# Kernel optimization log

Hardware: AMD Instinct MI355X
Metric: run time of the kernel (lower is better)

Reference implementation:

```python
import jax, jax.numpy as jnp
import numpy as np

N_SRC = 50000
N_DST = 50000
N_EDGES = 500000
HIDDEN = 128
HEADS = 8
HEAD_DIM = HIDDEN // HEADS
SCALE = HEAD_DIM ** -0.5


def setup_inputs() -> dict:
    key = jax.random.key(0)
    ks = jax.random.split(key, 12)
    lim = 1.0 / np.sqrt(HIDDEN)
    def lin(k):
        kw, kb = jax.random.split(k)
        W = jax.random.uniform(kw, (HIDDEN, HIDDEN), jnp.float32, -lim, lim)
        b = jax.random.uniform(kb, (HIDDEN,), jnp.float32, -lim, lim)
        return W, b
    Wq, bq = lin(ks[0]); Wk, bk = lin(ks[1]); Wv, bv = lin(ks[2]); Wo, bo = lin(ks[3])
    return {
        "x_src": jax.random.normal(ks[4], (N_SRC, HIDDEN), jnp.float32),
        "x_dst": jax.random.normal(ks[5], (N_DST, HIDDEN), jnp.float32),
        "edge_index": jax.random.randint(ks[6], (2, N_EDGES), 0, N_SRC, jnp.int64),
        "Wq": Wq, "bq": bq, "Wk": Wk, "bk": bk, "Wv": Wv, "bv": bv,
        "Wo": Wo, "bo": bo,
        "edge_bias": jax.random.normal(ks[7], (HEADS,), jnp.float32) * 0.02,
    }


def reference(x_src, x_dst, edge_index, Wq, bq, Wk, bk, Wv, bv, Wo, bo, edge_bias):
    num_dst = x_dst.shape[0]
    # projections (torch Linear: y = x W^T + b), reshape to (N, H, D)
    q = (x_dst @ Wq.T + bq).reshape(num_dst, HEADS, HEAD_DIM)
    k = (x_src @ Wk.T + bk).reshape(-1, HEADS, HEAD_DIM)
    v = (x_src @ Wv.T + bv).reshape(-1, HEADS, HEAD_DIM)
    src_idx, dst_idx = edge_index[0], edge_index[1]
    # per-edge dot-product scores: (E, H)
    scores = (q[dst_idx] * k[src_idx]).sum(-1) * SCALE + edge_bias
    # sparse softmax over edges grouped by destination
    m = jax.ops.segment_max(scores, dst_idx, num_segments=num_dst)  # (N_dst, H)
    e = jnp.exp(scores - m[dst_idx])
    s = jax.ops.segment_sum(e, dst_idx, num_segments=num_dst)  # (N_dst, H)
    w = e / (s[dst_idx] + 1e-8)  # (E, H)
    # scatter-add aggregate weighted values
    out = jax.ops.segment_sum(w[:, :, None] * v[src_idx], dst_idx, num_segments=num_dst)
    out = out.reshape(num_dst, HIDDEN)
    return out @ Wo.T + bo
```

## Files before the change

### kernel.cpp

```cpp
#include <hip/hip_runtime.h>
#include <math.h>

#define HIDDEN 128
#define SCALE 0.25f
#define NB_F 256

typedef __attribute__((ext_vector_type(8))) short short8v;
typedef __attribute__((ext_vector_type(4))) float f32x4;

__device__ __forceinline__ unsigned short f2bf(float f) {
  const unsigned u = __float_as_uint(f);
  const unsigned r = u + 0x7fffu + ((u >> 16) & 1u);
  return (unsigned short)(r >> 16);
}
__device__ __forceinline__ unsigned pack_bf2(float a, float b) {
  unsigned r;
  asm("v_cvt_pk_bf16_f32 %0, %1, %2" : "=v"(r) : "v"(a), "v"(b));
  return r;
}
__device__ __forceinline__ float bflo(unsigned u) { return __uint_as_float(u << 16); }
__device__ __forceinline__ float bfhi(unsigned u) { return __uint_as_float(u & 0xffff0000u); }

__device__ __forceinline__ void gload_lds16(const void* g, void* l) {
  __builtin_amdgcn_global_load_lds(
      (const __attribute__((address_space(1))) unsigned*)g,
      (__attribute__((address_space(3))) unsigned*)l, 16, 0, 0);
}

__global__ __launch_bounds__(256) void init_kernel(
    const float* __restrict__ W0, const float* __restrict__ W1,
    const float* __restrict__ W2, const float* __restrict__ W3,
    unsigned short* __restrict__ Wfrag, int* __restrict__ zero_base, int nzero4)
{
  if (blockIdx.x < 32) {
    const int chunk = blockIdx.x * 256 + threadIdx.x;
    const int m = chunk >> 11;
    const int rem = chunk & 2047;
    const int l = rem & 63;
    const int nkk = rem >> 6;
    const int n = nkk >> 2, kk = nkk & 3;
    const float* W = (m == 0) ? W0 : (m == 1) ? W1 : (m == 2) ? W2 : W3;
    const int row = n * 16 + (l & 15);
    const int k0 = kk * 32 + (l >> 4) * 8;
    const float4 v0 = *(const float4*)&W[row * 128 + k0];
    const float4 v1 = *(const float4*)&W[row * 128 + k0 + 4];
    uint4 o;
    o.x = (unsigned)f2bf(v0.x) | ((unsigned)f2bf(v0.y) << 16);
    o.y = (unsigned)f2bf(v0.z) | ((unsigned)f2bf(v0.w) << 16);
    o.z = (unsigned)f2bf(v1.x) | ((unsigned)f2bf(v1.y) << 16);
    o.w = (unsigned)f2bf(v1.z) | ((unsigned)f2bf(v1.w) << 16);
    *(uint4*)&Wfrag[(size_t)chunk * 8] = o;
  } else {
    const int idx4 = (blockIdx.x - 32) * 256 + threadIdx.x;
    if (idx4 < nzero4)
      *(int4*)&zero_base[idx4 * 4] = make_int4(0, 0, 0, 0);
  }
}

__global__ __launch_bounds__(256, 4) void qkv_count_kernel(
    const float* __restrict__ x_src, const float* __restrict__ x_dst,
    const unsigned short* __restrict__ Wfrag,
    const float* __restrict__ bq, const float* __restrict__ bk,
    const float* __restrict__ bv,
    unsigned short* __restrict__ qb, unsigned short* __restrict__ kvb,
    int Nsrc, int Ndst,
    const int* __restrict__ ei, int E, int* __restrict__ counts, int cblocks)
{
  __shared__ __align__(16) char WsB[32768];
  __shared__ float bias_s[128];
  const int t = threadIdx.x;
  int bid = blockIdx.x;

  if (bid < cblocks) {
    const int e = (bid * 256 + t) * 4;
    if (e + 4 <= E) {
      const int4 d = *(const int4*)&ei[E + e];
      atomicAdd(&counts[d.x], 1);
      atomicAdd(&counts[d.y], 1);
      atomicAdd(&counts[d.z], 1);
      atomicAdd(&counts[d.w], 1);
    } else {
      for (int k = e; k < E; ++k) atomicAdd(&counts[ei[E + k]], 1);
    }
    return;
  }
  bid -= cblocks;

  const int flavor = bid / NB_F, sub = bid % NB_F;
  const float* X; const float* bias; const unsigned short* wbase;
  unsigned short* out; int ostride, ooff, N;
  if (flavor == 0)      { X = x_src; bias = bk; wbase = Wfrag + 16384; out = kvb; ostride = 256; ooff = 0;   N = Nsrc; }
  else if (flavor == 1) { X = x_src; bias = bv; wbase = Wfrag + 32768; out = kvb; ostride = 256; ooff = 128; N = Nsrc; }
  else                  { X = x_dst; bias = bq; wbase = Wfrag;         out = qb;  ostride = 128; ooff = 0;   N = Ndst; }

  #pragma unroll
  for (int it = 0; it < 8; ++it) {
    const int off = (it * 256 + t) * 16;
    gload_lds16((const char*)wbase + off, WsB + off);
  }
  if (t < 128) bias_s[t] = bias[t];
  asm volatile("s_waitcnt vmcnt(0)" ::: "memory");
  __syncthreads();

  const int l = t & 63, w = t >> 6;
  const int r16 = l & 15, g16 = l >> 4;
  const int ntiles = (N + 15) >> 4;
  const int stride = NB_F * 4;
  int tile = sub * 4 + w;
  if (tile >= ntiles) return;

  float4 xv[8];
  {
    const int row = tile * 16 + r16;
    const bool valid = row < N;
    const float* xp = X + (size_t)row * 128 + g16 * 8;
    #pragma unroll
    for (int kk = 0; kk < 4; ++kk) {
      xv[2 * kk]     = valid ? *(const float4*)(xp + kk * 32)     : make_float4(0.f, 0.f, 0.f, 0.f);
      xv[2 * kk + 1] = valid ? *(const float4*)(xp + kk * 32 + 4) : make_float4(0.f, 0.f, 0.f, 0.f);
    }
  }
  for (; tile < ntiles; tile += stride) {
    const int nt = tile + stride;
    short8v a[4];
    #pragma unroll
    for (int kk = 0; kk < 4; ++kk) {
      uint4 u;
      u.x = pack_bf2(xv[2 * kk].x,     xv[2 * kk].y);
      u.y = pack_bf2(xv[2 * kk].z,     xv[2 * kk].w);
      u.z = pack_bf2(xv[2 * kk + 1].x, xv[2 * kk + 1].y);
      u.w = pack_bf2(xv[2 * kk + 1].z, xv[2 * kk + 1].w);
      a[kk] = *(short8v*)&u;
    }
    if (nt < ntiles) {
      const int row = nt * 16 + r16;
      const bool valid = row < N;
      const float* xp = X + (size_t)row * 128 + g16 * 8;
      #pragma unroll
      for (int kk = 0; kk < 4; ++kk) {
        xv[2 * kk]     = valid ? *(const float4*)(xp + kk * 32)     : make_float4(0.f, 0.f, 0.f, 0.f);
        xv[2 * kk + 1] = valid ? *(const float4*)(xp + kk * 32 + 4) : make_float4(0.f, 0.f, 0.f, 0.f);
      }
    }
    f32x4 acc[8];
    #pragma unroll
    for (int n = 0; n < 8; ++n) acc[n] = (f32x4){0.f, 0.f, 0.f, 0.f};
    #pragma unroll
    for (int kk = 0; kk < 4; ++kk) {
      #pragma unroll
      for (int n = 0; n < 8; ++n) {
        const short8v wf = *(const short8v*)&WsB[((n * 4 + kk) * 64 + l) * 16];
        acc[n] = __builtin_amdgcn_mfma_f32_16x16x32_bf16(wf, a[kk], acc[n], 0, 0, 0);
      }
    }
    const int row = tile * 16 + r16;
    if (row < N) {
      unsigned short* orow = out + (size_t)row * ostride + ooff;
      #pragma unroll
      for (int n = 0; n < 8; ++n) {
        const float4 bb = *(const float4*)&bias_s[n * 16 + g16 * 4];
        uint2 o;
        o.x = pack_bf2(acc[n][0] + bb.x, acc[n][1] + bb.y);
        o.y = pack_bf2(acc[n][2] + bb.z, acc[n][3] + bb.w);
        *(uint2*)&orow[n * 16 + g16 * 4] = o;
      }
    }
  }
}

__global__ __launch_bounds__(256, 4) void out_gemm_kernel(
    const unsigned short* __restrict__ agg, const unsigned short* __restrict__ Wfrag_o,
    const float* __restrict__ bo, float* __restrict__ Y, int N)
{
  __shared__ __align__(16) char WsB[32768];
  __shared__ float bias_s[128];
  const int t = threadIdx.x;
  #pragma unroll
  for (int it = 0; it < 8; ++it) {
    const int off = (it * 256 + t) * 16;
    gload_lds16((const char*)Wfrag_o + off, WsB + off);
  }
  if (t < 128) bias_s[t] = bo[t];
  asm volatile("s_waitcnt vmcnt(0)" ::: "memory");
  __syncthreads();

  const int l = t & 63, w = t >> 6;
  const int r16 = l & 15, g16 = l >> 4;
  const int ntiles = (N + 15) >> 4;
  const int stride = NB_F * 4;
  int tile = blockIdx.x * 4 + w;
  if (tile >= ntiles) return;

  uint4 av[4];
  {
    const int row = tile * 16 + r16;
    const bool valid = row < N;
    const unsigned short* ap = agg + (size_t)row * 128 + g16 * 8;
    #pragma unroll
    for (int kk = 0; kk < 4; ++kk)
      av[kk] = valid ? *(const uint4*)(ap + kk * 32) : make_uint4(0, 0, 0, 0);
  }
  for (; tile < ntiles; tile += stride) {
    const int nt = tile + stride;
    short8v a[4];
    #pragma unroll
    for (int kk = 0; kk < 4; ++kk) a[kk] = *(short8v*)&av[kk];
    if (nt < ntiles) {
      const int row = nt * 16 + r16;
      const bool valid = row < N;
      const unsigned short* ap = agg + (size_t)row * 128 + g16 * 8;
      #pragma unroll
      for (int kk = 0; kk < 4; ++kk)
        av[kk] = valid ? *(const uint4*)(ap + kk * 32) : make_uint4(0, 0, 0, 0);
    }
    f32x4 acc[8];
    #pragma unroll
    for (int n = 0; n < 8; ++n) acc[n] = (f32x4){0.f, 0.f, 0.f, 0.f};
    #pragma unroll
    for (int kk = 0; kk < 4; ++kk) {
      #pragma unroll
      for (int n = 0; n < 8; ++n) {
        const short8v wf = *(const short8v*)&WsB[((n * 4 + kk) * 64 + l) * 16];
        acc[n] = __builtin_amdgcn_mfma_f32_16x16x32_bf16(wf, a[kk], acc[n], 0, 0, 0);
      }
    }
    const int row = tile * 16 + r16;
    if (row < N) {
      float* yrow = Y + (size_t)row * 128;
      #pragma unroll
      for (int n = 0; n < 8; ++n) {
        const float4 bb = *(const float4*)&bias_s[n * 16 + g16 * 4];
        *(float4*)&yrow[n * 16 + g16 * 4] =
            make_float4(acc[n][0] + bb.x, acc[n][1] + bb.y, acc[n][2] + bb.z, acc[n][3] + bb.w);
      }
    }
  }
}

__global__ __launch_bounds__(256) void scan_fused_kernel(
    const int* __restrict__ counts, int n, int* __restrict__ bsums,
    int* __restrict__ done, int* __restrict__ offsets)
{
  const int b = blockIdx.x, t = threadIdx.x;
  const int lane = t & 63, wid = t >> 6;
  const int idx = b * 256 + t;
  const int x = (idx < n) ? counts[idx] : 0;
  int v = x;
  #pragma unroll
  for (int off = 1; off < 64; off <<= 1) {
    const int tmp = __shfl_up(v, off);
    if (lane >= off) v += tmp;
  }
  __shared__ int wsum[4];
  __shared__ int base_s;
  if (lane == 63) wsum[wid] = v;
  __syncthreads();
  if (t == 0) {
    bsums[b] = wsum[0] + wsum[1] + wsum[2] + wsum[3];
    __threadfence();
    atomicAdd(done, 1);
    while (atomicAdd(done, 0) < (int)gridDim.x) {}
  }
  __syncthreads();
  __threadfence();
  int pre = (t < b) ? bsums[t] : 0;
  #pragma unroll
  for (int off = 1; off < 64; off <<= 1) pre += __shfl_xor(pre, off);
  __shared__ int pres[4];
  if (lane == 0) pres[wid] = pre;
  __syncthreads();
  if (t == 0) base_s = pres[0] + pres[1] + pres[2] + pres[3];
  __syncthreads();
  int wbase = 0;
  for (int p = 0; p < wid; ++p) wbase += wsum[p];
  if (idx < n) offsets[idx] = base_s + wbase + v - x;
}

__global__ __launch_bounds__(256) void scatter_kernel(
    const int* __restrict__ ei, int E, int* __restrict__ offsets,
    int* __restrict__ csr_src)
{
  const int e = (blockIdx.x * 256 + threadIdx.x) * 4;
  if (e + 4 <= E) {
    const int4 s = *(const int4*)&ei[e];
    const int4 d = *(const int4*)&ei[E + e];
    int p;
    p = atomicAdd(&offsets[d.x], 1); csr_src[p] = s.x;
    p = atomicAdd(&offsets[d.y], 1); csr_src[p] = s.y;
    p = atomicAdd(&offsets[d.z], 1); csr_src[p] = s.z;
    p = atomicAdd(&offsets[d.w], 1); csr_src[p] = s.w;
  } else {
    for (int k = e; k < E; ++k) {
      const int d = ei[E + k];
      const int p = atomicAdd(&offsets[d], 1);
      csr_src[p] = ei[k];
    }
  }
}

__global__ __launch_bounds__(256) void edge_attn_kernel(
    const unsigned short* __restrict__ qb, const unsigned short* __restrict__ kvb,
    const float* __restrict__ eb, const int* __restrict__ offsets,
    const int* __restrict__ counts, const int* __restrict__ csr_src,
    unsigned short* __restrict__ agg, int Ndst)
{
  const int wave = blockIdx.x * 4 + (threadIdx.x >> 6);
  if (wave >= Ndst) return;
  const int lane = threadIdx.x & 63;
  const int eg = lane >> 3, h = lane & 7;

  const uint4 q0 = *(const uint4*)&qb[(size_t)wave * 128 + h * 16];
  const uint4 q1 = *(const uint4*)&qb[(size_t)wave * 128 + h * 16 + 8];
  const float bias = eb[h];
  const int ro = (wave == 0) ? 0 : offsets[wave - 1];
  const int cnt = counts[wave];

  float acc[16];
  #pragma unroll
  for (int j = 0; j < 16; ++j) acc[j] = 0.f;
  float s = 0.f;

  const int iters = (cnt + 7) >> 3;
  int eA = eg;
  bool actA = eA < cnt;
  int srcA = actA ? csr_src[ro + eA] : 0;
  size_t baseA = (size_t)srcA * 256 + h * 16;
  uint4 kA0 = *(const uint4*)&kvb[baseA];
  uint4 kA1 = *(const uint4*)&kvb[baseA + 8];
  uint4 vA0 = *(const uint4*)&kvb[baseA + 128];
  uint4 vA1 = *(const uint4*)&kvb[baseA + 136];
  int eB = eA + 8;
  bool actB = eB < cnt;
  int srcB = actB ? csr_src[ro + eB] : 0;

  for (int it = 0; it < iters; ++it) {
    const size_t baseB = (size_t)srcB * 256 + h * 16;
    const uint4 kB0 = *(const uint4*)&kvb[baseB];
    const uint4 kB1 = *(const uint4*)&kvb[baseB + 8];
    const uint4 vB0 = *(const uint4*)&kvb[baseB + 128];
    const uint4 vB1 = *(const uint4*)&kvb[baseB + 136];
    const int eC = eB + 8;
    const bool actC = eC < cnt;
    const int srcC = actC ? csr_src[ro + eC] : 0;

    float p = 0.f;
    p = fmaf(bflo(q0.x), bflo(kA0.x), p); p = fmaf(bfhi(q0.x), bfhi(kA0.x), p);
    p = fmaf(bflo(q0.y), bflo(kA0.y), p); p = fmaf(bfhi(q0.y), bfhi(kA0.y), p);
    p = fmaf(bflo(q0.z), bflo(kA0.z), p); p = fmaf(bfhi(q0.z), bfhi(kA0.z), p);
    p = fmaf(bflo(q0.w), bflo(kA0.w), p); p = fmaf(bfhi(q0.w), bfhi(kA0.w), p);
    p = fmaf(bflo(q1.x), bflo(kA1.x), p); p = fmaf(bfhi(q1.x), bfhi(kA1.x), p);
    p = fmaf(bflo(q1.y), bflo(kA1.y), p); p = fmaf(bfhi(q1.y), bfhi(kA1.y), p);
    p = fmaf(bflo(q1.z), bflo(kA1.z), p); p = fmaf(bfhi(q1.z), bfhi(kA1.z), p);
    p = fmaf(bflo(q1.w), bflo(kA1.w), p); p = fmaf(bfhi(q1.w), bfhi(kA1.w), p);

    const float wgt = actA ? __expf(fmaf(p, SCALE, bias)) : 0.f;
    s += wgt;
    acc[0]  = fmaf(wgt, bflo(vA0.x), acc[0]);  acc[1]  = fmaf(wgt, bfhi(vA0.x), acc[1]);
    acc[2]  = fmaf(wgt, bflo(vA0.y), acc[2]);  acc[3]  = fmaf(wgt, bfhi(vA0.y), acc[3]);
    acc[4]  = fmaf(wgt, bflo(vA0.z), acc[4]);  acc[5]  = fmaf(wgt, bfhi(vA0.z), acc[5]);
    acc[6]  = fmaf(wgt, bflo(vA0.w), acc[6]);  acc[7]  = fmaf(wgt, bfhi(vA0.w), acc[7]);
    acc[8]  = fmaf(wgt, bflo(vA1.x), acc[8]);  acc[9]  = fmaf(wgt, bfhi(vA1.x), acc[9]);
    acc[10] = fmaf(wgt, bflo(vA1.y), acc[10]); acc[11] = fmaf(wgt, bfhi(vA1.y), acc[11]);
    acc[12] = fmaf(wgt, bflo(vA1.z), acc[12]); acc[13] = fmaf(wgt, bfhi(vA1.z), acc[13]);
    acc[14] = fmaf(wgt, bflo(vA1.w), acc[14]); acc[15] = fmaf(wgt, bfhi(vA1.w), acc[15]);

    kA0 = kB0; kA1 = kB1; vA0 = vB0; vA1 = vB1;
    actA = actB; actB = actC; srcB = srcC; eB = eC;
  }

  const bool b0 = eg & 1, b1 = (eg >> 1) & 1, b2 = (eg >> 2) & 1;
  float r8[8];
  #pragma unroll
  for (int j = 0; j < 8; ++j) {
    const float keep = b0 ? acc[j + 8] : acc[j];
    const float send = b0 ? acc[j] : acc[j + 8];
    r8[j] = keep + __shfl_xor(send, 8);
  }
  float r4[4];
  #pragma unroll
  for (int j = 0; j < 4; ++j) {
    const float keep = b1 ? r8[j + 4] : r8[j];
    const float send = b1 ? r8[j] : r8[j + 4];
    r4[j] = keep + __shfl_xor(send, 16);
  }
  float r2[2];
  #pragma unroll
  for (int j = 0; j < 2; ++j) {
    const float keep = b2 ? r4[j + 2] : r4[j];
    const float send = b2 ? r4[j] : r4[j + 2];
    r2[j] = keep + __shfl_xor(send, 32);
  }
  s += __shfl_xor(s, 8); s += __shfl_xor(s, 16); s += __shfl_xor(s, 32);
  const float rs = 1.0f / (s + 1e-8f);
  const int col = h * 16 + (b0 ? 8 : 0) + (b1 ? 4 : 0) + (b2 ? 2 : 0);
  *(unsigned*)&agg[(size_t)wave * 128 + col] = pack_bf2(r2[0] * rs, r2[1] * rs);
}

extern "C" void kernel_launch(void* const* d_in, const int* in_sizes, int n_in,
                              void* d_out, int out_size, void* d_ws, size_t ws_size,
                              hipStream_t stream) {
  const float* x_src = (const float*)d_in[0];
  const float* x_dst = (const float*)d_in[1];
  const int*   ei    = (const int*)d_in[2];
  const float* Wq = (const float*)d_in[3];
  const float* bq = (const float*)d_in[4];
  const float* Wk = (const float*)d_in[5];
  const float* bk = (const float*)d_in[6];
  const float* Wv = (const float*)d_in[7];
  const float* bv = (const float*)d_in[8];
  const float* Wo = (const float*)d_in[9];
  const float* bo = (const float*)d_in[10];
  const float* eb = (const float*)d_in[11];

  const int Nsrc = in_sizes[0] / HIDDEN;
  const int Ndst = in_sizes[1] / HIDDEN;
  const int E    = in_sizes[2] / 2;

  char* w = (char*)d_ws;
  unsigned short* qb   = (unsigned short*)w; w += (size_t)Ndst * 128 * 2;
  unsigned short* kvb  = (unsigned short*)w; w += (size_t)Nsrc * 256 * 2;
  unsigned short* aggb = (unsigned short*)w; w += (size_t)Ndst * 128 * 2;
  unsigned short* Wb   = (unsigned short*)w; w += (size_t)4 * 16384 * 2;
  int* counts  = (int*)w; w += (size_t)Ndst * sizeof(int);
  int* done    = (int*)w; w += 64 * sizeof(int);
  int* offsets = (int*)w; w += (size_t)Ndst * sizeof(int);
  int* bsums   = (int*)w; w += 256 * sizeof(int);
  int* csr_src = (int*)w; w += (size_t)E * sizeof(int);

  dim3 blk256(256);
  const int nzero4 = (Ndst + 64 + 3) / 4;
  const int zblocks = (nzero4 + 255) / 256;
  init_kernel<<<32 + zblocks, blk256, 0, stream>>>(Wq, Wk, Wv, Wo, Wb, counts, nzero4);

  const int e4blocks = (E / 4 + 255) / 256;
  qkv_count_kernel<<<e4blocks + 3 * NB_F, blk256, 0, stream>>>(
      x_src, x_dst, Wb, bq, bk, bv, qb, kvb, Nsrc, Ndst, ei, E, counts, e4blocks);

  const int nb = (Ndst + 255) / 256;
  scan_fused_kernel<<<nb, blk256, 0, stream>>>(counts, Ndst, bsums, done, offsets);

  scatter_kernel<<<e4blocks, blk256, 0, stream>>>(ei, E, offsets, csr_src);

  const int ablocks = (Ndst + 3) / 4;
  edge_attn_kernel<<<ablocks, blk256, 0, stream>>>(qb, kvb, eb, offsets, counts,
                                                   csr_src, aggb, Ndst);

  out_gemm_kernel<<<NB_F, blk256, 0, stream>>>(aggb, Wb + 49152, bo, (float*)d_out, Ndst);
}
```

Before: 170.3 us.

## Keep weight fragments in registers and stage activations through swizzled double-buffered LDS

Both projection GEMM kernels now hold all 32 weight MFMA fragments in VGPRs instead of LDS. Activation tiles of 64 rows per block are staged through a double-buffered, XOR-swizzled LDS buffer: coalesced fp32 loads converted to bf16 for QKV, and global_load_lds for the output GEMM. Bias is folded into the accumulator init, and the edge-count blocks move after the GEMM blocks. The aim is to cut LDS weight reads and improve load coalescing, at the cost of higher register pressure (occupancy hint lowered from 4 to 2) and fewer GEMM blocks per type.

```diff
diff --git a/kernel.cpp b/kernel.cpp
--- a/kernel.cpp
+++ b/kernel.cpp
@@ -3,7 +3,8 @@
 
 #define HIDDEN 128
 #define SCALE 0.25f
-#define NB_F 256
+#define NB_TYPE 170
+#define NB_O 256
 
 typedef __attribute__((ext_vector_type(8))) short short8v;
 typedef __attribute__((ext_vector_type(4))) float f32x4;
@@ -57,22 +58,21 @@
   }
 }
 
-__global__ __launch_bounds__(256, 4) void qkv_count_kernel(
+__global__ __launch_bounds__(256, 2) void qkv_gemm_count_kernel(
     const float* __restrict__ x_src, const float* __restrict__ x_dst,
     const unsigned short* __restrict__ Wfrag,
     const float* __restrict__ bq, const float* __restrict__ bk,
     const float* __restrict__ bv,
     unsigned short* __restrict__ qb, unsigned short* __restrict__ kvb,
     int Nsrc, int Ndst,
-    const int* __restrict__ ei, int E, int* __restrict__ counts, int cblocks)
-{
-  __shared__ __align__(16) char WsB[32768];
-  __shared__ float bias_s[128];
+    const int* __restrict__ ei, int E, int* __restrict__ counts)
+{
+  __shared__ __align__(16) char Xs[2][16384];
   const int t = threadIdx.x;
   int bid = blockIdx.x;
 
-  if (bid < cblocks) {
-    const int e = (bid * 256 + t) * 4;
+  if (bid >= 3 * NB_TYPE) {
+    const int e = ((bid - 3 * NB_TYPE) * 256 + t) * 4;
     if (e + 4 <= E) {
       const int4 d = *(const int4*)&ei[E + e];
       atomicAdd(&counts[d.x], 1);
@@ -84,156 +84,156 @@
     }
     return;
   }
-  bid -= cblocks;
-
-  const int flavor = bid / NB_F, sub = bid % NB_F;
+
+  const int l = t & 63, w = t >> 6;
+  const int r16 = l & 15, g16 = l >> 4;
+
   const float* X; const float* bias; const unsigned short* wbase;
   unsigned short* out; int ostride, ooff, N;
-  if (flavor == 0)      { X = x_src; bias = bk; wbase = Wfrag + 16384; out = kvb; ostride = 256; ooff = 0;   N = Nsrc; }
-  else if (flavor == 1) { X = x_src; bias = bv; wbase = Wfrag + 32768; out = kvb; ostride = 256; ooff = 128; N = Nsrc; }
-  else                  { X = x_dst; bias = bq; wbase = Wfrag;         out = qb;  ostride = 128; ooff = 0;   N = Ndst; }
-
-  #pragma unroll
-  for (int it = 0; it < 8; ++it) {
-    const int off = (it * 256 + t) * 16;
-    gload_lds16((const char*)wbase + off, WsB + off);
-  }
-  if (t < 128) bias_s[t] = bias[t];
-  asm volatile("s_waitcnt vmcnt(0)" ::: "memory");
-  __syncthreads();
-
+  if (bid < NB_TYPE)          { X = x_src; bias = bk; wbase = Wfrag + 16384; out = kvb; ostride = 256; ooff = 0;   N = Nsrc; }
+  else if (bid < 2 * NB_TYPE) { bid -= NB_TYPE;   X = x_src; bias = bv; wbase = Wfrag + 32768; out = kvb; ostride = 256; ooff = 128; N = Nsrc; }
+  else                        { bid -= 2 * NB_TYPE; X = x_dst; bias = bq; wbase = Wfrag;       out = qb;  ostride = 128; ooff = 0;   N = Ndst; }
+  const int ntiles = (N + 63) >> 6;
+
+  short8v wfr[32];
+  #pragma unroll
+  for (int i = 0; i < 32; ++i) wfr[i] = ((const short8v*)wbase)[i * 64 + l];
+
+  const int srow = l >> 5;
+  const int scol = (l & 31) * 4;
+
+  float4 xv[8];
+  int tile = bid;
+  {
+    #pragma unroll
+    for (int j = 0; j < 8; ++j) {
+      const int r = j * 2 + srow;
+      const int g = tile * 64 + w * 16 + r;
+      xv[j] = make_float4(0.f, 0.f, 0.f, 0.f);
+      if (g < N) xv[j] = *(const float4*)&X[(size_t)g * 128 + scol];
+    }
+    #pragma unroll
+    for (int j = 0; j < 8; ++j) {
+      const int r = j * 2 + srow;
+      uint2 p;
+      p.x = pack_bf2(xv[j].x, xv[j].y);
+      p.y = pack_bf2(xv[j].z, xv[j].w);
+      *(uint2*)&Xs[0][(w * 16 + r) * 256 + ((scol * 2) ^ ((r & 7) << 4))] = p;
+    }
+  }
+  int cur = 0;
+  for (; tile < ntiles; tile += NB_TYPE) {
+    const int nt = tile + NB_TYPE;
+    if (nt < ntiles) {
+      #pragma unroll
+      for (int j = 0; j < 8; ++j) {
+        const int r = j * 2 + srow;
+        const int g = nt * 64 + w * 16 + r;
+        xv[j] = make_float4(0.f, 0.f, 0.f, 0.f);
+        if (g < N) xv[j] = *(const float4*)&X[(size_t)g * 128 + scol];
+      }
+    }
+    f32x4 acc[8];
+    #pragma unroll
+    for (int n = 0; n < 8; ++n) {
+      const float4 bb = *(const float4*)&bias[n * 16 + g16 * 4];
+      acc[n] = (f32x4){bb.x, bb.y, bb.z, bb.w};
+    }
+    const char* ax = &Xs[cur][(w * 16 + r16) * 256];
+    #pragma unroll
+    for (int kk = 0; kk < 4; ++kk) {
+      const short8v b = *(const short8v*)(ax + ((kk * 64 + g16 * 16) ^ ((r16 & 7) << 4)));
+      #pragma unroll
+      for (int n = 0; n < 8; ++n)
+        acc[n] = __builtin_amdgcn_mfma_f32_16x16x32_bf16(wfr[n * 4 + kk], b, acc[n], 0, 0, 0);
+    }
+    const int grow = tile * 64 + w * 16 + r16;
+    if (grow < N) {
+      unsigned short* orow = out + (size_t)grow * ostride + ooff;
+      #pragma unroll
+      for (int n = 0; n < 8; ++n) {
+        uint2 o;
+        o.x = pack_bf2(acc[n][0], acc[n][1]);
+        o.y = pack_bf2(acc[n][2], acc[n][3]);
+        *(uint2*)&orow[n * 16 + g16 * 4] = o;
+      }
+    }
+    if (nt < ntiles) {
+      #pragma unroll
+      for (int j = 0; j < 8; ++j) {
+        const int r = j * 2 + srow;
+        uint2 p;
+        p.x = pack_bf2(xv[j].x, xv[j].y);
+        p.y = pack_bf2(xv[j].z, xv[j].w);
+        *(uint2*)&Xs[cur ^ 1][(w * 16 + r) * 256 + ((scol * 2) ^ ((r & 7) << 4))] = p;
+      }
+    }
+    cur ^= 1;
+  }
+}
+
+__global__ __launch_bounds__(256, 2) void out_gemm_kernel(
+    const unsigned short* __restrict__ agg, const unsigned short* __restrict__ Wo_frag,
+    const float* __restrict__ bo, float* __restrict__ Y, int N)
+{
+  __shared__ __align__(16) char Xs[2][16384];
+  const int t = threadIdx.x;
   const int l = t & 63, w = t >> 6;
   const int r16 = l & 15, g16 = l >> 4;
-  const int ntiles = (N + 15) >> 4;
-  const int stride = NB_F * 4;
-  int tile = sub * 4 + w;
-  if (tile >= ntiles) return;
-
-  float4 xv[8];
+  const int ntiles = (N + 63) >> 6;
+
+  short8v wfr[32];
+  #pragma unroll
+  for (int i = 0; i < 32; ++i) wfr[i] = ((const short8v*)Wo_frag)[i * 64 + l];
+
+  int tile = blockIdx.x;
   {
-    const int row = tile * 16 + r16;
-    const bool valid = row < N;
-    const float* xp = X + (size_t)row * 128 + g16 * 8;
+    #pragma unroll
+    for (int it = 0; it < 4; ++it) {
+      const int row16 = it * 4 + (l >> 4);
+      const int grow = tile * 64 + w * 16 + row16;
+      const int sb = ((l & 15) * 16) ^ ((row16 & 7) << 4);
+      gload_lds16((const char*)agg + (size_t)grow * 256 + sb,
+                  &Xs[0][w * 4096 + it * 1024 + l * 16]);
+    }
+  }
+  int cur = 0;
+  for (; tile < ntiles; tile += NB_O) {
+    const int nt = tile + NB_O;
+    asm volatile("s_waitcnt vmcnt(0)" ::: "memory");
+    __builtin_amdgcn_sched_barrier(0);
+    if (nt < ntiles) {
+      #pragma unroll
+      for (int it = 0; it < 4; ++it) {
+        const int row16 = it * 4 + (l >> 4);
+        const int grow = nt * 64 + w * 16 + row16;
+        const int sb = ((l & 15) * 16) ^ ((row16 & 7) << 4);
+        gload_lds16((const char*)agg + (size_t)grow * 256 + sb,
+                    &Xs[cur ^ 1][w * 4096 + it * 1024 + l * 16]);
+      }
+    }
+    f32x4 acc[8];
+    #pragma unroll
+    for (int n = 0; n < 8; ++n) {
+      const float4 bb = *(const float4*)&bo[n * 16 + g16 * 4];
+      acc[n] = (f32x4){bb.x, bb.y, bb.z, bb.w};
+    }
+    const char* ax = &Xs[cur][(w * 16 + r16) * 256];
     #pragma unroll
     for (int kk = 0; kk < 4; ++kk) {
-      xv[2 * kk]     = valid ? *(const float4*)(xp + kk * 32)     : make_float4(0.f, 0.f, 0.f, 0.f);
-      xv[2 * kk + 1] = valid ? *(const float4*)(xp + kk * 32 + 4) : make_float4(0.f, 0.f, 0.f, 0.f);
-    }
-  }
-  for (; tile < ntiles; tile += stride) {
-    const int nt = tile + stride;
-    short8v a[4];
-    #pragma unroll
-    for (int kk = 0; kk < 4; ++kk) {
-      uint4 u;
-      u.x = pack_bf2(xv[2 * kk].x,     xv[2 * kk].y);
-      u.y = pack_bf2(xv[2 * kk].z,     xv[2 * kk].w);
-      u.z = pack_bf2(xv[2 * kk + 1].x, xv[2 * kk + 1].y);
-      u.w = pack_bf2(xv[2 * kk + 1].z, xv[2 * kk + 1].w);
-      a[kk] = *(short8v*)&u;
-    }
-    if (nt < ntiles) {
-      const int row = nt * 16 + r16;
-      const bool valid = row < N;
-      const float* xp = X + (size_t)row * 128 + g16 * 8;
-      #pragma unroll
-      for (int kk = 0; kk < 4; ++kk) {
-        xv[2 * kk]     = valid ? *(const float4*)(xp + kk * 32)     : make_float4(0.f, 0.f, 0.f, 0.f);
-        xv[2 * kk + 1] = valid ? *(const float4*)(xp + kk * 32 + 4) : make_float4(0.f, 0.f, 0.f, 0.f);
-      }
-    }
-    f32x4 acc[8];
-    #pragma unroll
-    for (int n = 0; n < 8; ++n) acc[n] = (f32x4){0.f, 0.f, 0.f, 0.f};
-    #pragma unroll
-    for (int kk = 0; kk < 4; ++kk) {
-      #pragma unroll
-      for (int n = 0; n < 8; ++n) {
-        const short8v wf = *(const short8v*)&WsB[((n * 4 + kk) * 64 + l) * 16];
-        acc[n] = __builtin_amdgcn_mfma_f32_16x16x32_bf16(wf, a[kk], acc[n], 0, 0, 0);
-      }
-    }
-    const int row = tile * 16 + r16;
-    if (row < N) {
-      unsigned short* orow = out + (size_t)row * ostride + ooff;
-      #pragma unroll
-      for (int n = 0; n < 8; ++n) {
-        const float4 bb = *(const float4*)&bias_s[n * 16 + g16 * 4];
-        uint2 o;
-        o.x = pack_bf2(acc[n][0] + bb.x, acc[n][1] + bb.y);
-        o.y = pack_bf2(acc[n][2] + bb.z, acc[n][3] + bb.w);
-        *(uint2*)&orow[n * 16 + g16 * 4] = o;
-      }
-    }
-  }
-}
-
-__global__ __launch_bounds__(256, 4) void out_gemm_kernel(
-    const unsigned short* __restrict__ agg, const unsigned short* __restrict__ Wfrag_o,
-    const float* __restrict__ bo, float* __restrict__ Y, int N)
-{
-  __shared__ __align__(16) char WsB[32768];
-  __shared__ float bias_s[128];
-  const int t = threadIdx.x;
-  #pragma unroll
-  for (int it = 0; it < 8; ++it) {
-    const int off = (it * 256 + t) * 16;
-    gload_lds16((const char*)Wfrag_o + off, WsB + off);
-  }
-  if (t < 128) bias_s[t] = bo[t];
-  asm volatile("s_waitcnt vmcnt(0)" ::: "memory");
-  __syncthreads();
-
-  const int l = t & 63, w = t >> 6;
-  const int r16 = l & 15, g16 = l >> 4;
-  const int ntiles = (N + 15) >> 4;
-  const int stride = NB_F * 4;
-  int tile = blockIdx.x * 4 + w;
-  if (tile >= ntiles) return;
-
-  uint4 av[4];
-  {
-    const int row = tile * 16 + r16;
-    const bool valid = row < N;
-    const unsigned short* ap = agg + (size_t)row * 128 + g16 * 8;
-    #pragma unroll
-    for (int kk = 0; kk < 4; ++kk)
-      av[kk] = valid ? *(const uint4*)(ap + kk * 32) : make_uint4(0, 0, 0, 0);
-  }
-  for (; tile < ntiles; tile += stride) {
-    const int nt = tile + stride;
-    short8v a[4];
-    #pragma unroll
-    for (int kk = 0; kk < 4; ++kk) a[kk] = *(short8v*)&av[kk];
-    if (nt < ntiles) {
-      const int row = nt * 16 + r16;
-      const bool valid = row < N;
-      const unsigned short* ap = agg + (size_t)row * 128 + g16 * 8;
-      #pragma unroll
-      for (int kk = 0; kk < 4; ++kk)
-        av[kk] = valid ? *(const uint4*)(ap + kk * 32) : make_uint4(0, 0, 0, 0);
-    }
-    f32x4 acc[8];
-    #pragma unroll
-    for (int n = 0; n < 8; ++n) acc[n] = (f32x4){0.f, 0.f, 0.f, 0.f};
-    #pragma unroll
-    for (int kk = 0; kk < 4; ++kk) {
-      #pragma unroll
-      for (int n = 0; n < 8; ++n) {
-        const short8v wf = *(const short8v*)&WsB[((n * 4 + kk) * 64 + l) * 16];
-        acc[n] = __builtin_amdgcn_mfma_f32_16x16x32_bf16(wf, a[kk], acc[n], 0, 0, 0);
-      }
-    }
-    const int row = tile * 16 + r16;
-    if (row < N) {
-      float* yrow = Y + (size_t)row * 128;
-      #pragma unroll
-      for (int n = 0; n < 8; ++n) {
-        const float4 bb = *(const float4*)&bias_s[n * 16 + g16 * 4];
-        *(float4*)&yrow[n * 16 + g16 * 4] =
-            make_float4(acc[n][0] + bb.x, acc[n][1] + bb.y, acc[n][2] + bb.z, acc[n][3] + bb.w);
-      }
-    }
+      const short8v b = *(const short8v*)(ax + ((kk * 64 + g16 * 16) ^ ((r16 & 7) << 4)));
+      #pragma unroll
+      for (int n = 0; n < 8; ++n)
+        acc[n] = __builtin_amdgcn_mfma_f32_16x16x32_bf16(wfr[n * 4 + kk], b, acc[n], 0, 0, 0);
+    }
+    const int grow = tile * 64 + w * 16 + r16;
+    if (grow < N) {
+      float* yrow = Y + (size_t)grow * 128;
+      #pragma unroll
+      for (int n = 0; n < 8; ++n)
+        *(float4*)&yrow[n * 16 + g16 * 4] = make_float4(acc[n][0], acc[n][1], acc[n][2], acc[n][3]);
+    }
+    cur ^= 1;
   }
 }
 
@@ -433,8 +433,8 @@
   init_kernel<<<32 + zblocks, blk256, 0, stream>>>(Wq, Wk, Wv, Wo, Wb, counts, nzero4);
 
   const int e4blocks = (E / 4 + 255) / 256;
-  qkv_count_kernel<<<e4blocks + 3 * NB_F, blk256, 0, stream>>>(
-      x_src, x_dst, Wb, bq, bk, bv, qb, kvb, Nsrc, Ndst, ei, E, counts, e4blocks);
+  qkv_gemm_count_kernel<<<3 * NB_TYPE + e4blocks, blk256, 0, stream>>>(
+      x_src, x_dst, Wb, bq, bk, bv, qb, kvb, Nsrc, Ndst, ei, E, counts);
 
   const int nb = (Ndst + 255) / 256;
   scan_fused_kernel<<<nb, blk256, 0, stream>>>(counts, Ndst, bsums, done, offsets);
@@ -445,5 +445,5 @@
   edge_attn_kernel<<<ablocks, blk256, 0, stream>>>(qb, kvb, eb, offsets, counts,
                                                    csr_src, aggb, Ndst);
 
-  out_gemm_kernel<<<NB_F, blk256, 0, stream>>>(aggb, Wb + 49152, bo, (float*)d_out, Ndst);
-}
+  out_gemm_kernel<<<NB_O, blk256, 0, stream>>>(aggb, Wb + 49152, bo, (float*)d_out, Ndst);
+}
```

Result: faster. 155.7 us (-8.5%).
